# Performance work log

Hardware: AMD Instinct MI355X
Metric: run time of the kernel (lower is better)

The kernel has to match this reference:

```python
import jax, jax.numpy as jnp
import numpy as np

N_NODES = 100000
N_EDGES = 800000
D = 128


def setup_inputs() -> dict:
    key = jax.random.key(0)
    ks = jax.random.split(key, 6)
    x = jax.random.normal(ks[0], (N_NODES, D), dtype=jnp.float32)
    src = jax.random.randint(ks[1], (N_EDGES,), 0, N_NODES, dtype=jnp.int64 if jax.config.jax_enable_x64 else jnp.int32)
    dst = jax.random.randint(ks[2], (N_EDGES,), 0, N_NODES, dtype=jnp.int64 if jax.config.jax_enable_x64 else jnp.int32)
    W_self = jax.random.normal(ks[3], (D, D), dtype=jnp.float32) / np.sqrt(D)
    W_neigh = jax.random.normal(ks[4], (D, D), dtype=jnp.float32) / np.sqrt(D)
    b = jax.random.normal(ks[5], (D,), dtype=jnp.float32) * 0.01
    return {"x": x, "src": src, "dst": dst, "W_self": W_self, "W_neigh": W_neigh, "b": b}


def reference(x, src, dst, W_self, W_neigh, b):
    # DGL SAGEConv('mean'): mean-aggregate source features over incoming edges.
    msgs = x[src]  # [E, D] gather (irregular)
    sums = jax.ops.segment_sum(msgs, dst, num_segments=N_NODES)  # [N, D]
    deg = jax.ops.segment_sum(jnp.ones((msgs.shape[0],), dtype=x.dtype), dst,
                              num_segments=N_NODES)
    # DGL clamps in-degree to at least 1 (zero-in-degree nodes get zero h_neigh).
    h_neigh = sums / jnp.maximum(deg, 1.0)[:, None]
    # rst = fc_self(h) + fc_neigh(h_neigh) + bias, then ReLU activation.
    out = x @ W_self + h_neigh @ W_neigh + b
    return jax.nn.relu(out)
```

## Files before the change

### kernel.cpp

```cpp
#include <hip/hip_runtime.h>
#include <stdint.h>

#define N_NODES 100000
#define N_EDGES 800000
#define D 128

typedef _Float16 f16x8 __attribute__((ext_vector_type(8)));
typedef float f32x4 __attribute__((ext_vector_type(4)));


__global__ void hist_rank(const int* __restrict__ dst, int* __restrict__ cnt,
                          int* __restrict__ rank) {
    int e = blockIdx.x * blockDim.x + threadIdx.x;
    if (e < N_EDGES) rank[e] = atomicAdd(&cnt[dst[e]], 1);
}

__global__ void scan_local(const int* __restrict__ cnt, int* __restrict__ offsets,
                           int* __restrict__ bs) {
    __shared__ int sdata[256];
    const int t = threadIdx.x;
    const int base = blockIdx.x * 1024 + t * 4;
    int v[4];
    int s = 0;
#pragma unroll
    for (int j = 0; j < 4; ++j) {
        int i = base + j;
        v[j] = (i < N_NODES) ? cnt[i] : 0;
        s += v[j];
    }
    sdata[t] = s;
    __syncthreads();
    int incl = s;
    for (int off = 1; off < 256; off <<= 1) {
        int add = (t >= off) ? sdata[t - off] : 0;
        __syncthreads();
        incl += add;
        sdata[t] = incl;
        __syncthreads();
    }
    int run = incl - s;
#pragma unroll
    for (int j = 0; j < 4; ++j) {
        int i = base + j;
        if (i < N_NODES) offsets[i] = run;
        run += v[j];
    }
    if (t == 255) bs[blockIdx.x] = incl;
}

__global__ void scan_block2(int* __restrict__ bs, int* __restrict__ offsets, int nblk) {
    int t = threadIdx.x;
    int v0 = (2 * t < nblk) ? bs[2 * t] : 0;
    int v1 = (2 * t + 1 < nblk) ? bs[2 * t + 1] : 0;
    int s = v0 + v1;
    int incl = s;
    for (int off = 1; off < 64; off <<= 1) {
        int n = __shfl_up(incl, off, 64);
        if (t >= off) incl += n;
    }
    int excl = incl - s;
    if (2 * t < nblk) bs[2 * t] = excl;
    if (2 * t + 1 < nblk) bs[2 * t + 1] = excl + v0;
    if (t == 63) offsets[N_NODES] = incl;
}

__global__ void scan_add(int* __restrict__ offsets, const int* __restrict__ bs) {
    const int t = threadIdx.x;
    const int base = blockIdx.x * 1024 + t * 4;
    const int add = bs[blockIdx.x];
#pragma unroll
    for (int j = 0; j < 4; ++j) {
        int i = base + j;
        if (i < N_NODES) offsets[i] += add;
    }
}

__global__ void scatter2(const int* __restrict__ src, const int* __restrict__ dst,
                         const int* __restrict__ offsets, const int* __restrict__ rank,
                         int* __restrict__ esrc) {
    int e = blockIdx.x * blockDim.x + threadIdx.x;
    if (e < N_EDGES) esrc[offsets[dst[e]] + rank[e]] = src[e];
}

__global__ __launch_bounds__(256) void gemm_reg(const float* __restrict__ x,
                                                const float* __restrict__ Ws,
                                                const float* __restrict__ Wn,
                                                const float* __restrict__ bias,
                                                float* __restrict__ pre,
                                                _Float16* __restrict__ y2) {
    const int half = blockIdx.x & 1;
    const int bid = blockIdx.x >> 1;
    const int nb = gridDim.x >> 1;
    const int tid = threadIdx.x;
    const int w = tid >> 6;
    const int lane = tid & 63;
    const int lr = lane & 15;
    const int lk = (lane >> 4) * 8;
    const int wc = w & 1;
    const int ws_ = w >> 1;

    const float* __restrict__ W = half ? Wn : Ws;

    f16x8 bfrag[4][4];
#pragma unroll
    for (int ks = 0; ks < 4; ++ks) {
#pragma unroll
        for (int fc = 0; fc < 4; ++fc) {
            const int col = wc * 64 + fc * 16 + lr;
            const int kb = ks * 32 + lk;
            f16x8 h;
#pragma unroll
            for (int j = 0; j < 8; ++j) h[j] = (_Float16)W[(long)(kb + j) * D + col];
            bfrag[ks][fc] = h;
        }
    }
    float bv[4];
    if (half == 0) {
#pragma unroll
        for (int fc = 0; fc < 4; ++fc) bv[fc] = bias[wc * 64 + fc * 16 + lr];
    }

    const int nstrip = N_NODES / 16;
    for (int s = bid * 2 + ws_; s < nstrip; s += nb * 2) {
        const float* __restrict__ xr = &x[(long)(s * 16 + lr) * D];
        f32x4 a0[4], a1[4];
#pragma unroll
        for (int ks = 0; ks < 4; ++ks) {
            a0[ks] = *(const f32x4*)&xr[ks * 32 + lk];
            a1[ks] = *(const f32x4*)&xr[ks * 32 + lk + 4];
        }
        f32x4 acc[4];
#pragma unroll
        for (int fc = 0; fc < 4; ++fc) acc[fc] = (f32x4){0.f, 0.f, 0.f, 0.f};
#pragma unroll
        for (int ks = 0; ks < 4; ++ks) {
            f16x8 af;
#pragma unroll
            for (int j = 0; j < 4; ++j) {
                af[j] = (_Float16)a0[ks][j];
                af[4 + j] = (_Float16)a1[ks][j];
            }
#pragma unroll
            for (int fc = 0; fc < 4; ++fc)
                acc[fc] = __builtin_amdgcn_mfma_f32_16x16x32_f16(af, bfrag[ks][fc],
                                                                 acc[fc], 0, 0, 0);
        }
        const int rb = s * 16 + (lane >> 4) * 4;
        if (half == 0) {
#pragma unroll
            for (int fc = 0; fc < 4; ++fc) {
                const int col = wc * 64 + fc * 16 + lr;
#pragma unroll
                for (int i = 0; i < 4; ++i)
                    pre[(long)(rb + i) * D + col] = acc[fc][i] + bv[fc];
            }
        } else {
#pragma unroll
            for (int fc = 0; fc < 4; ++fc) {
                const int col = wc * 64 + fc * 16 + lr;
#pragma unroll
                for (int i = 0; i < 4; ++i)
                    y2[(long)(rb + i) * D + col] = (_Float16)acc[fc][i];
            }
        }
    }
}

__global__ __launch_bounds__(256) void agg_ep(const _Float16* __restrict__ y2,
                                              const int* __restrict__ offsets,
                                              const int* __restrict__ esrc,
                                              float* __restrict__ out) {
    __shared__ float red[16][128];
    const int n = blockIdx.x;
    const int slot = threadIdx.x >> 4;
    const int c8 = threadIdx.x & 15;
    const int s = offsets[n];
    const int e = offsets[n + 1];
    float a[8] = {0.f, 0.f, 0.f, 0.f, 0.f, 0.f, 0.f, 0.f};
    for (int j = s + slot; j < e; j += 16) {
        int sn = esrc[j];
        f16x8 v = *(const f16x8*)&y2[(long)sn * D + c8 * 8];
#pragma unroll
        for (int i = 0; i < 8; ++i) a[i] += (float)v[i];
    }
    *(float4*)&red[slot][c8 * 8] = make_float4(a[0], a[1], a[2], a[3]);
    *(float4*)&red[slot][c8 * 8 + 4] = make_float4(a[4], a[5], a[6], a[7]);
    __syncthreads();
    if (threadIdx.x < 128) {
        const int d = threadIdx.x;
        float ssum = 0.f;
#pragma unroll
        for (int r = 0; r < 16; ++r) ssum += red[r][d];
        int deg = e - s;
        float v = out[(long)n * D + d];
        if (deg > 0) v += ssum / (float)deg;
        out[(long)n * D + d] = fmaxf(v, 0.f);
    }
}


extern "C" void kernel_launch(void* const* d_in, const int* in_sizes, int n_in,
                              void* d_out, int out_size, void* d_ws, size_t ws_size,
                              hipStream_t stream) {
    const float* x  = (const float*)d_in[0];
    const int* src  = (const int*)d_in[1];
    const int* dst  = (const int*)d_in[2];
    const float* Ws = (const float*)d_in[3];
    const float* Wn = (const float*)d_in[4];
    const float* b  = (const float*)d_in[5];
    float* out = (float*)d_out;

    int* cnt     = (int*)d_ws;
    int* offsets = cnt + N_NODES;
    int* bs      = offsets + N_NODES + 1;
    int* rank    = bs + 128;
    int* esrc    = rank + N_EDGES;
    uintptr_t p = (uintptr_t)(esrc + N_EDGES);
    p = (p + 255) & ~(uintptr_t)255;
    _Float16* y2 = (_Float16*)p;

    const int nblk_scan = (N_NODES + 1023) / 1024;

    hipMemsetAsync(cnt, 0, N_NODES * sizeof(int), stream);
    hist_rank<<<(N_EDGES + 255) / 256, 256, 0, stream>>>(dst, cnt, rank);
    scan_local<<<nblk_scan, 256, 0, stream>>>(cnt, offsets, bs);
    scan_block2<<<1, 64, 0, stream>>>(bs, offsets, nblk_scan);
    scan_add<<<nblk_scan, 256, 0, stream>>>(offsets, bs);
    scatter2<<<(N_EDGES + 255) / 256, 256, 0, stream>>>(src, dst, offsets, rank, esrc);
    gemm_reg<<<2048, 256, 0, stream>>>(x, Ws, Wn, b, out, y2);
    agg_ep<<<N_NODES, 256, 0, stream>>>(y2, offsets, esrc, out);
}
```

Measured before the change: 280.0 us.

## Assign one wavefront per node in aggregation with shuffle reduction

The aggregation kernel now handles four nodes per 256-thread block, one wavefront per node, instead of one node per block. Each wave processes four edges at a time across 16 lanes of 8 halfs, reduces partial sums with cross-lane xor shuffles instead of shared memory plus __syncthreads, and writes the epilogue with vectorized float4 stores. This targets the launch and occupancy overhead of 100k blocks with mostly idle threads (average degree 8) and the shared-memory reduction, at the cost of less edge parallelism for high-degree nodes.

```diff
diff --git a/kernel.cpp b/kernel.cpp
--- a/kernel.cpp
+++ b/kernel.cpp
@@ -166,35 +166,44 @@
     }
 }
 
-__global__ __launch_bounds__(256) void agg_ep(const _Float16* __restrict__ y2,
-                                              const int* __restrict__ offsets,
-                                              const int* __restrict__ esrc,
-                                              float* __restrict__ out) {
-    __shared__ float red[16][128];
-    const int n = blockIdx.x;
-    const int slot = threadIdx.x >> 4;
-    const int c8 = threadIdx.x & 15;
+__global__ __launch_bounds__(256) void agg_wave(const _Float16* __restrict__ y2,
+                                                const int* __restrict__ offsets,
+                                                const int* __restrict__ esrc,
+                                                float* __restrict__ out) {
+    const int n = blockIdx.x * 4 + (threadIdx.x >> 6);
+    const int lane = threadIdx.x & 63;
+    const int slot = lane >> 4;
+    const int c8 = lane & 15;
     const int s = offsets[n];
     const int e = offsets[n + 1];
     float a[8] = {0.f, 0.f, 0.f, 0.f, 0.f, 0.f, 0.f, 0.f};
-    for (int j = s + slot; j < e; j += 16) {
+    for (int j = s + slot; j < e; j += 4) {
         int sn = esrc[j];
         f16x8 v = *(const f16x8*)&y2[(long)sn * D + c8 * 8];
 #pragma unroll
         for (int i = 0; i < 8; ++i) a[i] += (float)v[i];
     }
-    *(float4*)&red[slot][c8 * 8] = make_float4(a[0], a[1], a[2], a[3]);
-    *(float4*)&red[slot][c8 * 8 + 4] = make_float4(a[4], a[5], a[6], a[7]);
-    __syncthreads();
-    if (threadIdx.x < 128) {
-        const int d = threadIdx.x;
-        float ssum = 0.f;
-#pragma unroll
-        for (int r = 0; r < 16; ++r) ssum += red[r][d];
-        int deg = e - s;
-        float v = out[(long)n * D + d];
-        if (deg > 0) v += ssum / (float)deg;
-        out[(long)n * D + d] = fmaxf(v, 0.f);
+#pragma unroll
+    for (int i = 0; i < 8; ++i) {
+        a[i] += __shfl_xor(a[i], 16, 64);
+        a[i] += __shfl_xor(a[i], 32, 64);
+    }
+    if (slot == 0) {
+        const int deg = e - s;
+        const float inv = (deg > 0) ? 1.f / (float)deg : 0.f;
+        float4 p0 = *(const float4*)&out[(long)n * D + c8 * 8];
+        float4 p1 = *(const float4*)&out[(long)n * D + c8 * 8 + 4];
+        float4 o0, o1;
+        o0.x = fmaxf(p0.x + a[0] * inv, 0.f);
+        o0.y = fmaxf(p0.y + a[1] * inv, 0.f);
+        o0.z = fmaxf(p0.z + a[2] * inv, 0.f);
+        o0.w = fmaxf(p0.w + a[3] * inv, 0.f);
+        o1.x = fmaxf(p1.x + a[4] * inv, 0.f);
+        o1.y = fmaxf(p1.y + a[5] * inv, 0.f);
+        o1.z = fmaxf(p1.z + a[6] * inv, 0.f);
+        o1.w = fmaxf(p1.w + a[7] * inv, 0.f);
+        *(float4*)&out[(long)n * D + c8 * 8] = o0;
+        *(float4*)&out[(long)n * D + c8 * 8 + 4] = o1;
     }
 }
 
@@ -228,5 +237,5 @@
     scan_add<<<nblk_scan, 256, 0, stream>>>(offsets, bs);
     scatter2<<<(N_EDGES + 255) / 256, 256, 0, stream>>>(src, dst, offsets, rank, esrc);
     gemm_reg<<<2048, 256, 0, stream>>>(x, Ws, Wn, b, out, y2);
-    agg_ep<<<N_NODES, 256, 0, stream>>>(y2, offsets, esrc, out);
-}
+    agg_wave<<<N_NODES / 4, 256, 0, stream>>>(y2, offsets, esrc, out);
+}
```

Measured after the change: 252.2 us. -9.9%, faster.
